# Kernel tuning notes

Hardware: AMD Instinct MI355X
Metric: run time of the kernel (lower is better)

Reference implementation:

```python
import jax, jax.numpy as jnp
import numpy as np

EPS = 1e-5
INF = 1e5


def setup_inputs() -> dict:
    key = jax.random.key(0)
    ks = iter(jax.random.split(key, 32))
    B, N, F, H, NH, C = 2, 384, 64, 64, 4, 32
    def lin(k, fi, fo):
        return jax.random.normal(k, (fi, fo), jnp.float32) / np.sqrt(fi).astype(np.float32)
    d = {}
    d['h'] = jax.random.normal(next(ks), (B, N, F), jnp.float32)
    d['x'] = jax.random.normal(next(ks), (B, N, 3), jnp.float32)
    # edge_model (ConcatenationFilter): Linear(2F+1,H), SiLU, Linear(H,H), SiLU
    d['We0'] = lin(next(ks), 2 * F + 1, H); d['be0'] = jnp.zeros(H, jnp.float32)
    d['We1'] = lin(next(ks), H, H);         d['be1'] = jnp.zeros(H, jnp.float32)
    # semantic_attention_mlp: Linear(H, n_heads), LeakyReLU(0.2)
    d['Ws'] = lin(next(ks), H, NH);         d['bs'] = jnp.zeros(NH, jnp.float32)
    # coefficients_mlp: Linear(H,H), SiLU, Linear(H,C)
    d['Wc0'] = lin(next(ks), H, H);         d['bc0'] = jnp.zeros(H, jnp.float32)
    d['Wc1'] = lin(next(ks), H, C);         d['bc1'] = jnp.zeros(C, jnp.float32)
    # post_norm_mlp: Linear(C,H), SiLU, Linear(H,H)
    d['Wp0'] = lin(next(ks), C, H);         d['bp0'] = jnp.zeros(H, jnp.float32)
    d['Wp1'] = lin(next(ks), H, H);         d['bp1'] = jnp.zeros(H, jnp.float32)
    # coordinate_mlp: Linear(H,H), SiLU, Linear(H,1,bias=False) init gain 1e-3
    d['Wx0'] = lin(next(ks), H, H);         d['bx0'] = jnp.zeros(H, jnp.float32)
    d['Wx1'] = lin(next(ks), H, 1) * 1e-3
    # node_mlp: Linear(NH*H + H + F, H), SiLU, Linear(H, F)
    d['Wn0'] = lin(next(ks), NH * H + H + F, H); d['bn0'] = jnp.zeros(H, jnp.float32)
    d['Wn1'] = lin(next(ks), H, F);         d['bn1'] = jnp.zeros(F, jnp.float32)
    d['log_gamma'] = jnp.zeros(NH, jnp.float32)
    return d


def _forward(h, x, We0, be0, We1, be1, Ws, bs, Wc0, bc0, Wc1, bc1,
             Wp0, bp0, Wp1, bp1, Wx0, bx0, Wx1, Wn0, bn0, Wn1, bn1, log_gamma):
    B, N, F = h.shape
    silu = jax.nn.silu

    # pairwise displacements and distances: (B,N,N,3), (B,N,N,1)
    x_minus_xt = x[:, :, None, :] - x[:, None, :, :]
    norm = jnp.sqrt(jnp.sum(x_minus_xt * x_minus_xt, axis=-1, keepdims=True) + EPS)

    # pairwise node-feature concat + distance -> edge MLP (ConcatenationFilter)
    hi = jnp.broadcast_to(h[:, :, None, :], (B, N, N, F))
    hj = jnp.broadcast_to(h[:, None, :, :], (B, N, N, F))
    e_in = jnp.concatenate([hi, hj, norm], axis=-1)           # (B,N,N,2F+1)
    h_e = silu(silu(e_in @ We0 + be0) @ We1 + be1)            # (B,N,N,H)

    eye = jnp.eye(N, dtype=h.dtype)[None, :, :, None]         # mask self-edges

    # euclidean attention per head, softmax over neighbors j (axis=-2)
    eu = jax.nn.softmax(-(norm + INF * eye) * jnp.exp(log_gamma), axis=-2)  # (B,N,N,NH)
    # semantic attention
    sem_logits = jax.nn.leaky_relu(h_e @ Ws + bs, 0.2) - INF * eye
    sem = jax.nn.softmax(sem_logits, axis=-2)                 # (B,N,N,NH)
    comb = eu * sem
    comb = comb / (jnp.sum(comb, axis=-2, keepdims=True) + EPS)

    # attention-weighted multi-head edge features, aggregated over neighbors
    h_e_att = (comb[..., :, None] * h_e[..., None, :]).reshape(B, N, N, -1)  # (B,N,N,NH*H)
    h_e_agg = jnp.sum(h_e_att, axis=-2)                       # (B,N,NH*H)

    # spatial attention: equivariant combinations of unit direction vectors
    coeff = silu(h_e @ Wc0 + bc0) @ Wc1 + bc1                 # (B,N,N,C)
    x_hat = x_minus_xt / (norm + EPS)                         # (B,N,N,3)
    combinations = coeff[..., :, None] * x_hat[..., None, :]  # (B,N,N,C,3)
    comb_sum = jnp.mean(combinations, axis=2)                 # mean over j -> (B,N,C,3)
    comb_norm = jnp.sum(comb_sum * comb_sum, axis=-1)         # (B,N,C)
    h_comb = silu(comb_norm @ Wp0 + bp0) @ Wp1 + bp1          # (B,N,H)

    # node update (residual)
    node_in = jnp.concatenate([h, h_e_agg, h_comb], axis=-1)
    h_out = h + (silu(node_in @ Wn0 + bn0) @ Wn1 + bn1)

    # coordinate update: scalar-gated displacements, mean over neighbors
    scale = silu(h_e @ Wx0 + bx0) @ Wx1                       # (B,N,N,1)
    x_out = x + jnp.mean(x_minus_xt * scale, axis=2)          # (B,N,3)
    return h_out, x_out


def reference(h, x, We0, be0, We1, be1, Ws, bs, Wc0, bc0, Wc1, bc1,
              Wp0, bp0, Wp1, bp1, Wx0, bx0, Wx1, Wn0, bn0, Wn1, bn1, log_gamma):
    return _forward(h, x, We0, be0, We1, be1, Ws, bs, Wc0, bc0, Wc1, bc1,
                    Wp0, bp0, Wp1, bp1, Wx0, bx0, Wx1, Wn0, bn0, Wn1, bn1, log_gamma)
```

## Files before the change

### kernel.cpp

```cpp
#include <hip/hip_runtime.h>

#define NPT 384
#define NB 2
#define HOFF 49152

typedef unsigned short u16;
typedef unsigned int u32;
typedef __bf16 bf16x8 __attribute__((ext_vector_type(8)));
typedef float f32x4 __attribute__((ext_vector_type(4)));

struct alignas(16) U4 { u32 x, y, z, w; };

constexpr float kEPS = 1e-5f;
constexpr float kINF = 1e5f;

__device__ __forceinline__ u16 f2b(float f) {
  u32 x = __float_as_uint(f);
  x += 0x7fffu + ((x >> 16) & 1u);
  return (u16)(x >> 16);
}
__device__ __forceinline__ float b2f(u32 u) { return __uint_as_float(u << 16); }
__device__ __forceinline__ float silu_f(float v) { return v / (1.f + __expf(-v)); }
__device__ __forceinline__ float wredmax(float v) {
#pragma unroll
  for (int m = 32; m >= 1; m >>= 1) v = fmaxf(v, __shfl_xor(v, m, 64));
  return v;
}
__device__ __forceinline__ float wredsum(float v) {
#pragma unroll
  for (int m = 32; m >= 1; m >>= 1) v += __shfl_xor(v, m, 64);
  return v;
}
__device__ __forceinline__ void up8(U4 u, float* f) {
  f[0] = b2f(u.x & 0xffffu); f[1] = b2f(u.x >> 16);
  f[2] = b2f(u.y & 0xffffu); f[3] = b2f(u.y >> 16);
  f[4] = b2f(u.z & 0xffffu); f[5] = b2f(u.z >> 16);
  f[6] = b2f(u.w & 0xffffu); f[7] = b2f(u.w >> 16);
}

__global__ __launch_bounds__(64) void sake_prep(
    const float* __restrict__ h, const float* __restrict__ We0,
    const float* __restrict__ be0, const float* __restrict__ We1,
    const float* __restrict__ Wc0, const float* __restrict__ Wc1,
    const float* __restrict__ Wx0, const float* __restrict__ Ws,
    float* __restrict__ U, float* __restrict__ V, u16* __restrict__ WT)
{
  const int t = threadIdx.x;
  const int blk = blockIdx.x;
  if (blk < NB * NPT) {
    __shared__ float hs[64];
    hs[t] = h[blk * 64 + t];
    __syncthreads();
    float u = be0[t], v = 0.f;
#pragma unroll 8
    for (int k = 0; k < 64; k++) {
      float hv = hs[k];
      u = fmaf(hv, We0[k * 64 + t], u);
      v = fmaf(hv, We0[(64 + k) * 64 + t], v);
    }
    U[blk * 64 + t] = u;
    V[blk * 64 + t] = v;
  } else {
    const int wsel = blk - NB * NPT;
    if (wsel == 4) {
      u16* dst = WT + 14336;
      for (int o = t; o < 16 * 64; o += 64) {
        int c = o >> 6, k = o & 63;
        dst[o] = (c < 4) ? f2b(Ws[k * 4 + c]) : (u16)0;
      }
      return;
    }
    const float* src; int nout; u16* dst;
    if      (wsel == 0) { src = We1; nout = 64; dst = WT;         }
    else if (wsel == 1) { src = Wc0; nout = 64; dst = WT + 4096;  }
    else if (wsel == 2) { src = Wx0; nout = 64; dst = WT + 8192;  }
    else                { src = Wc1; nout = 32; dst = WT + 12288; }
    const int total = 64 * nout;
    for (int o = t; o < total; o += 64) {
      int n = o >> 6, k = o & 63;
      dst[o] = f2b(src[k * nout + n]);
    }
  }
}

struct MainArgs {
  const float *h, *x, *U, *V;
  const u16 *We1T, *Wc0T, *Wx0T, *Wc1T, *WsPT;
  const float *We0, *bs, *be1, *bc0, *bc1, *bx0, *Wx1, *log_gamma;
  const float *Wp0, *bp0, *Wp1, *bp1, *Wn0, *bn0, *Wn1, *bn1;
  float* out;
};

template<bool DUALT>
__device__ __forceinline__ void gemm64(const u16* aT, const u16* __restrict__ wG,
                                       const float* bias, u16* oT, u16* oTT, int w, int lane)
{
  const int m0 = w << 4;
  const int arow = m0 + (lane & 15);
  const int r7 = arow & 7;
  const int kg = lane >> 4;
  bf16x8 a0 = *(const bf16x8*)(aT + arow * 64 + ((kg ^ r7) << 3));
  bf16x8 a1 = *(const bf16x8*)(aT + arow * 64 + ((((kg + 4)) ^ r7) << 3));
#pragma unroll
  for (int nt = 0; nt < 4; nt++) {
    const int col = (nt << 4) + (lane & 15);
    const u16* wrow = wG + col * 64;
    bf16x8 b0 = *(const bf16x8*)(wrow + (kg << 3));
    bf16x8 b1 = *(const bf16x8*)(wrow + 32 + (kg << 3));
    f32x4 acc = {0.f, 0.f, 0.f, 0.f};
    acc = __builtin_amdgcn_mfma_f32_16x16x32_bf16(a0, b0, acc, 0, 0, 0);
    acc = __builtin_amdgcn_mfma_f32_16x16x32_bf16(a1, b1, acc, 0, 0, 0);
    const float bv = bias[col];
    const int cs = col >> 3, ce = col & 7;
#pragma unroll
    for (int r = 0; r < 4; r++) {
      const int row = m0 + (kg << 2) + r;
      const u16 v = f2b(silu_f(acc[r] + bv));
      oT[row * 64 + ((cs ^ (row & 7)) << 3) + ce] = v;
      if constexpr (DUALT)
        oTT[col * 64 + ((((row >> 3)) ^ (col & 7)) << 3) + (row & 7)] = v;
    }
  }
}

__global__ __launch_bounds__(256, 3) void sake_main(MainArgs A)
{
  __shared__ __align__(16) u16 buf0[64 * 64];
  __shared__ __align__(16) u16 hes[64 * 64];
  __shared__ __align__(16) u16 hesT[64 * 64];
  __shared__ __align__(16) u16 E_lds[16 * 64];
  __shared__ __align__(16) u16 coeff[64 * 34];
  __shared__ float raw_lds[64 * 5];
  __shared__ float disp[64][3];
  __shared__ float nrm_s[64];
  __shared__ float invn_s[64];
  __shared__ float sU[64], wd[64], sbe1[64], sbc0[64], sbx0[64], sWx1[64];
  __shared__ float sbc1[32], sbs[4], sgam[4], xi_s[3];
  __shared__ float facL_s[4], coefh_s[4];
  __shared__ float node_in[384];
  __shared__ float t0s[64];
  __shared__ float cmv[96];

  const int t = threadIdx.x;
  const int w = t >> 6, lane = t & 63;
  const int bi = blockIdx.x;
  const int b = bi / NPT, i = bi - b * NPT;
  const int jj2 = t >> 2, q4 = t & 3;

  if (t < 64) {
    sU[t]   = A.U[bi * 64 + t];
    wd[t]   = A.We0[128 * 64 + t];
    sbe1[t] = A.be1[t];
    sbc0[t] = A.bc0[t];
    sbx0[t] = A.bx0[t];
    sWx1[t] = A.Wx1[t];
    if (t < 32) sbc1[t] = A.bc1[t];
    if (t < 4) { sbs[t] = A.bs[t]; sgam[t] = __expf(A.log_gamma[t]); }
    if (t < 3) xi_s[t] = A.x[(b * NPT + i) * 3 + t];
  }
  ((u32*)E_lds)[t] = 0; ((u32*)E_lds)[256 + t] = 0;
  __syncthreads();

  f32x4 aFrag = {0.f, 0.f, 0.f, 0.f};
  float mL = -1e30f, SL = 0.f, mb = -1e30f, Sb = 0.f, saPart = 0.f;
  float cA0 = 0, cA1 = 0, cA2 = 0, xA0 = 0, xA1 = 0, xA2 = 0;

  for (int jt = 0; jt < 6; ++jt) {
    const int j0 = jt << 6;
    __syncthreads();

    {
      const int j = j0 + jj2;
      const float* xp = &A.x[(b * NPT + j) * 3];
      float dx0 = xi_s[0] - xp[0], dx1 = xi_s[1] - xp[1], dx2 = xi_s[2] - xp[2];
      float nr = sqrtf(fmaf(dx0, dx0, fmaf(dx1, dx1, fmaf(dx2, dx2, kEPS))));
      if (q4 == 0) {
        disp[jj2][0] = dx0; disp[jj2][1] = dx1; disp[jj2][2] = dx2;
        nrm_s[jj2] = nr; invn_s[jj2] = 1.f / (nr + kEPS);
      }
      const float4* vp = (const float4*)(A.V + (size_t)(b * NPT + j) * 64 + q4 * 16);
      float4 v0_ = vp[0], v1_ = vp[1], v2_ = vp[2], v3_ = vp[3];
      float vv[16] = {v0_.x, v0_.y, v0_.z, v0_.w, v1_.x, v1_.y, v1_.z, v1_.w,
                      v2_.x, v2_.y, v2_.z, v2_.w, v3_.x, v3_.y, v3_.z, v3_.w};
      u16 pk[16];
#pragma unroll
      for (int e = 0; e < 16; e++) {
        const int f = q4 * 16 + e;
        pk[e] = f2b(silu_f(sU[f] + vv[e] + nr * wd[f]));
      }
      U4 lo, hi;
      lo.x = pk[0] | ((u32)pk[1] << 16);  lo.y = pk[2] | ((u32)pk[3] << 16);
      lo.z = pk[4] | ((u32)pk[5] << 16);  lo.w = pk[6] | ((u32)pk[7] << 16);
      hi.x = pk[8] | ((u32)pk[9] << 16);  hi.y = pk[10] | ((u32)pk[11] << 16);
      hi.z = pk[12] | ((u32)pk[13] << 16); hi.w = pk[14] | ((u32)pk[15] << 16);
      const int r7 = jj2 & 7;
      *(U4*)(buf0 + jj2 * 64 + (((q4 * 2) ^ r7) << 3)) = lo;
      *(U4*)(buf0 + jj2 * 64 + (((q4 * 2 + 1) ^ r7) << 3)) = hi;
    }
    gemm64<true>(buf0, A.We1T, sbe1, hes, hesT, w, lane);
    __syncthreads();

    gemm64<false>(hes, A.Wc0T, sbc0, buf0, nullptr, w, lane);
    {
      const int m0 = w << 4;
      const int arow = m0 + (lane & 15);
      const int r7a = arow & 7;
      const int kg = lane >> 4;
      bf16x8 a0 = *(const bf16x8*)(buf0 + arow * 64 + ((kg ^ r7a) << 3));
      bf16x8 a1 = *(const bf16x8*)(buf0 + arow * 64 + (((kg + 4) ^ r7a) << 3));
#pragma unroll
      for (int nt = 0; nt < 2; nt++) {
        const int col = (nt << 4) + (lane & 15);
        const u16* wrow = A.Wc1T + col * 64;
        bf16x8 b0 = *(const bf16x8*)(wrow + (kg << 3));
        bf16x8 b1 = *(const bf16x8*)(wrow + 32 + (kg << 3));
        f32x4 acc = {0.f, 0.f, 0.f, 0.f};
        acc = __builtin_amdgcn_mfma_f32_16x16x32_bf16(a0, b0, acc, 0, 0, 0);
        acc = __builtin_amdgcn_mfma_f32_16x16x32_bf16(a1, b1, acc, 0, 0, 0);
        const float bv = sbc1[col];
#pragma unroll
        for (int r = 0; r < 4; r++) {
          const int row = m0 + (kg << 2) + r;
          coeff[row * 34 + col] = f2b(acc[r] + bv);
        }
      }
    }
    {
      const int c = t & 31, g = t >> 5;
#pragma unroll
      for (int it = 0; it < 8; ++it) {
        const int jj = (g << 3) + it;
        const float s = b2f(coeff[jj * 34 + c]) * invn_s[jj];
        cA0 = fmaf(s, disp[jj][0], cA0);
        cA1 = fmaf(s, disp[jj][1], cA1);
        cA2 = fmaf(s, disp[jj][2], cA2);
      }
    }
    gemm64<false>(hes, A.Wx0T, sbx0, buf0, nullptr, w, lane);
    {
      const int jj = jj2;
      const int r7 = jj & 7;
      float acc = 0.f;
#pragma unroll
      for (int c2 = 0; c2 < 2; c2++) {
        const int c = q4 * 2 + c2;
        U4 u = *(const U4*)(buf0 + jj * 64 + ((c ^ r7) << 3));
        float f8[8]; up8(u, f8);
#pragma unroll
        for (int e = 0; e < 8; e++) acc = fmaf(f8[e], sWx1[c * 8 + e], acc);
      }
      acc += __shfl_xor(acc, 1, 64);
      acc += __shfl_xor(acc, 2, 64);
      if (q4 == 0) {
        xA0 = fmaf(disp[jj][0], acc, xA0);
        xA1 = fmaf(disp[jj][1], acc, xA1);
        xA2 = fmaf(disp[jj][2], acc, xA2);
      }
    }
    {
      const int m0 = w << 4;
      const int arow = m0 + (lane & 15);
      const int r7a = arow & 7;
      const int kg = lane >> 4;
      bf16x8 a0 = *(const bf16x8*)(hes + arow * 64 + ((kg ^ r7a) << 3));
      bf16x8 a1 = *(const bf16x8*)(hes + arow * 64 + (((kg + 4) ^ r7a) << 3));
      const u16* wrow = A.WsPT + (lane & 15) * 64;
      bf16x8 b0 = *(const bf16x8*)(wrow + (kg << 3));
      bf16x8 b1 = *(const bf16x8*)(wrow + 32 + (kg << 3));
      f32x4 acc = {0.f, 0.f, 0.f, 0.f};
      acc = __builtin_amdgcn_mfma_f32_16x16x32_bf16(a0, b0, acc, 0, 0, 0);
      acc = __builtin_amdgcn_mfma_f32_16x16x32_bf16(a1, b1, acc, 0, 0, 0);
      if ((lane & 15) < 4) {
#pragma unroll
        for (int r = 0; r < 4; r++)
          raw_lds[(m0 + (kg << 2) + r) * 5 + (lane & 15)] = acc[r];
      }
    }
    __syncthreads();

    {
      const int jj = lane, head = w;
      float raw = raw_lds[jj * 5 + head] + sbs[head];
      float bsem = (raw > 0.f) ? raw : 0.2f * raw;
      const bool self = (j0 + jj) == i;
      if (self) bsem -= kINF;
      const float aeu = -(nrm_s[jj] + (self ? kINF : 0.f)) * sgam[head];
      const float L = aeu + bsem;
      const float nmb = fmaxf(mb, wredmax(bsem));
      const float nmL = fmaxf(mL, wredmax(L));
      saPart += __expf(aeu);
      const float eB = __expf(bsem - nmb);
      const float eL = __expf(L - nmL);
      Sb = fmaf(Sb, __expf(mb - nmb), wredsum(eB));
      const float facL = __expf(mL - nmL);
      SL = fmaf(SL, facL, wredsum(eL));
      mb = nmb; mL = nmL;
      E_lds[head * 64 + (((jj >> 3) ^ head) << 3) + (jj & 7)] = f2b(eL);
      if (lane == 0) facL_s[head] = facL;
    }
    __syncthreads();

    {
      const int kg = lane >> 4;
      const int erow = lane & 15;
      const int e7 = erow & 7;
      bf16x8 ea0 = *(const bf16x8*)(E_lds + erow * 64 + ((kg ^ e7) << 3));
      bf16x8 ea1 = *(const bf16x8*)(E_lds + erow * 64 + (((kg + 4) ^ e7) << 3));
      const int f = (w << 4) + (lane & 15);
      const int f7 = f & 7;
      bf16x8 hb0 = *(const bf16x8*)(hesT + f * 64 + ((kg ^ f7) << 3));
      bf16x8 hb1 = *(const bf16x8*)(hesT + f * 64 + (((kg + 4) ^ f7) << 3));
#pragma unroll
      for (int r = 0; r < 4; r++) aFrag[r] *= facL_s[r];
      aFrag = __builtin_amdgcn_mfma_f32_16x16x32_bf16(ea0, hb0, aFrag, 0, 0, 0);
      aFrag = __builtin_amdgcn_mfma_f32_16x16x32_bf16(ea1, hb1, aFrag, 0, 0, 0);
    }
  }

  __syncthreads();
  float* scratch = (float*)coeff;
  float* xscr = (float*)hes;
  scratch[t * 3 + 0] = cA0; scratch[t * 3 + 1] = cA1; scratch[t * 3 + 2] = cA2;
  if (q4 == 0) { xscr[jj2 * 3 + 0] = xA0; xscr[jj2 * 3 + 1] = xA1; xscr[jj2 * 3 + 2] = xA2; }
  {
    const float Sa = wredsum(saPart);
    if (lane == 0) {
      const float Ff = __expf(mL - mb);
      const float denom = fmaf(SL, Ff, kEPS * Sa * Sb);
      coefh_s[w] = Ff / denom;
    }
  }
  if (t < 64) node_in[t] = A.h[bi * 64 + t];
  __syncthreads();
  if (lane < 16) {
#pragma unroll
    for (int r = 0; r < 4; r++)
      node_in[64 + r * 64 + (w << 4) + lane] = aFrag[r] * coefh_s[r];
  }
  if (t < 96) {
    const int c = t & 31, d = t >> 5;
    float s = 0.f;
#pragma unroll
    for (int g = 0; g < 8; g++) s += scratch[(g * 32 + c) * 3 + d];
    cmv[d * 32 + c] = s * (1.f / 384.f);
  }
  if (t >= 128 && t < 131) {
    const int d = t - 128;
    float s = 0.f;
    for (int k = 0; k < 64; k++) s += xscr[k * 3 + d];
    A.out[HOFF + bi * 3 + d] = xi_s[d] + s * (1.f / 384.f);
  }
  __syncthreads();
  if (t < 32) {
    float v0 = cmv[t], v1 = cmv[32 + t], v2 = cmv[64 + t];
    nrm_s[t] = v0 * v0 + v1 * v1 + v2 * v2;
  }
  __syncthreads();
  if (t < 64) {
    float acc = A.bp0[t];
    for (int c = 0; c < 32; c++) acc = fmaf(nrm_s[c], A.Wp0[c * 64 + t], acc);
    t0s[t] = silu_f(acc);
  }
  __syncthreads();
  if (t < 64) {
    float acc = A.bp1[t];
    for (int k = 0; k < 64; k++) acc = fmaf(t0s[k], A.Wp1[k * 64 + t], acc);
    node_in[320 + t] = acc;
  }
  __syncthreads();
  {
    const int f = t & 63, q = t >> 6;
    float acc = 0.f;
    const int k0 = q * 96;
    for (int k = 0; k < 96; k++) acc = fmaf(node_in[k0 + k], A.Wn0[(k0 + k) * 64 + f], acc);
    scratch[q * 64 + f] = acc;
  }
  __syncthreads();
  if (t < 64) {
    float s = scratch[t] + scratch[64 + t] + scratch[128 + t] + scratch[192 + t] + A.bn0[t];
    t0s[t] = silu_f(s);
  }
  __syncthreads();
  if (t < 64) {
    float acc = A.bn1[t];
    for (int k = 0; k < 64; k++) acc = fmaf(t0s[k], A.Wn1[k * 64 + t], acc);
    A.out[bi * 64 + t] = A.h[bi * 64 + t] + acc;
  }
}

extern "C" void kernel_launch(void* const* d_in, const int* in_sizes, int n_in,
                              void* d_out, int out_size, void* d_ws, size_t ws_size,
                              hipStream_t stream)
{
  (void)in_sizes; (void)n_in; (void)out_size; (void)ws_size;
  const float* h   = (const float*)d_in[0];
  const float* x   = (const float*)d_in[1];
  const float* We0 = (const float*)d_in[2];
  const float* be0 = (const float*)d_in[3];
  const float* We1 = (const float*)d_in[4];
  const float* be1 = (const float*)d_in[5];
  const float* Ws  = (const float*)d_in[6];
  const float* bs  = (const float*)d_in[7];
  const float* Wc0 = (const float*)d_in[8];
  const float* bc0 = (const float*)d_in[9];
  const float* Wc1 = (const float*)d_in[10];
  const float* bc1 = (const float*)d_in[11];
  const float* Wp0 = (const float*)d_in[12];
  const float* bp0 = (const float*)d_in[13];
  const float* Wp1 = (const float*)d_in[14];
  const float* bp1 = (const float*)d_in[15];
  const float* Wx0 = (const float*)d_in[16];
  const float* bx0 = (const float*)d_in[17];
  const float* Wx1 = (const float*)d_in[18];
  const float* Wn0 = (const float*)d_in[19];
  const float* bn0 = (const float*)d_in[20];
  const float* Wn1 = (const float*)d_in[21];
  const float* bn1 = (const float*)d_in[22];
  const float* lg  = (const float*)d_in[23];

  float* U = (float*)d_ws;
  float* V = U + NB * NPT * 64;
  u16* WT = (u16*)(V + NB * NPT * 64);

  sake_prep<<<NB * NPT + 5, 64, 0, stream>>>(h, We0, be0, We1, Wc0, Wc1, Wx0, Ws, U, V, WT);

  MainArgs A;
  A.h = h; A.x = x; A.U = U; A.V = V;
  A.We1T = WT; A.Wc0T = WT + 4096; A.Wx0T = WT + 8192; A.Wc1T = WT + 12288;
  A.WsPT = WT + 14336;
  A.We0 = We0; A.bs = bs; A.be1 = be1; A.bc0 = bc0; A.bc1 = bc1;
  A.bx0 = bx0; A.Wx1 = Wx1; A.log_gamma = lg;
  A.Wp0 = Wp0; A.bp0 = bp0; A.Wp1 = Wp1; A.bp1 = bp1;
  A.Wn0 = Wn0; A.bn0 = bn0; A.Wn1 = Wn1; A.bn1 = bn1;
  A.out = (float*)d_out;

  sake_main<<<NB * NPT, 256, 0, stream>>>(A);
}
```

Before: 118.6 us.

## Split neighbor tiles across blocks with partial softmax records and merge kernel

Instead of each block looping over all six 64-neighbor tiles for one node, each block now processes a single (node, tile) pair and writes partial attention sums, softmax max/sum statistics, coefficient and coordinate partials to a workspace record. A new merge kernel combines the per-tile records with log-sum-exp rescaling and runs the post-norm and node MLPs. This raises grid size sixfold and drops LDS use so more blocks fit per CU, at the cost of an extra launch, global round-trips for partials, and repeated per-block setup. It also switches to hardware bf16 conversion and rcp-based SiLU.

```diff
diff --git a/kernel.cpp b/kernel.cpp
--- a/kernel.cpp
+++ b/kernel.cpp
@@ -2,7 +2,11 @@
 
 #define NPT 384
 #define NB 2
+#define NROW (NB*NPT)
+#define NT 6
 #define HOFF 49152
+#define RECB 1024
+#define REC_OFF 424960
 
 typedef unsigned short u16;
 typedef unsigned int u32;
@@ -14,13 +18,10 @@
 constexpr float kEPS = 1e-5f;
 constexpr float kINF = 1e5f;
 
-__device__ __forceinline__ u16 f2b(float f) {
-  u32 x = __float_as_uint(f);
-  x += 0x7fffu + ((x >> 16) & 1u);
-  return (u16)(x >> 16);
-}
+__device__ __forceinline__ u16 f2b(float f) { __bf16 b = (__bf16)f; return __builtin_bit_cast(u16, b); }
+__device__ __forceinline__ u32 pk2(float lo, float hi) { return (u32)f2b(lo) | ((u32)f2b(hi) << 16); }
 __device__ __forceinline__ float b2f(u32 u) { return __uint_as_float(u << 16); }
-__device__ __forceinline__ float silu_f(float v) { return v / (1.f + __expf(-v)); }
+__device__ __forceinline__ float silu_f(float v) { return v * __builtin_amdgcn_rcpf(1.f + __expf(-v)); }
 __device__ __forceinline__ float wredmax(float v) {
 #pragma unroll
   for (int m = 32; m >= 1; m >>= 1) v = fmaxf(v, __shfl_xor(v, m, 64));
@@ -47,7 +48,7 @@
 {
   const int t = threadIdx.x;
   const int blk = blockIdx.x;
-  if (blk < NB * NPT) {
+  if (blk < NROW) {
     __shared__ float hs[64];
     hs[t] = h[blk * 64 + t];
     __syncthreads();
@@ -61,7 +62,7 @@
     U[blk * 64 + t] = u;
     V[blk * 64 + t] = v;
   } else {
-    const int wsel = blk - NB * NPT;
+    const int wsel = blk - NROW;
     if (wsel == 4) {
       u16* dst = WT + 14336;
       for (int o = t; o < 16 * 64; o += 64) {
@@ -84,11 +85,10 @@
 }
 
 struct MainArgs {
-  const float *h, *x, *U, *V;
+  const float *x, *U, *V;
   const u16 *We1T, *Wc0T, *Wx0T, *Wc1T, *WsPT;
   const float *We0, *bs, *be1, *bc0, *bc1, *bx0, *Wx1, *log_gamma;
-  const float *Wp0, *bp0, *Wp1, *bp1, *Wn0, *bn0, *Wn1, *bn1;
-  float* out;
+  char* rec;
 };
 
 template<bool DUALT>
@@ -123,29 +123,35 @@
   }
 }
 
-__global__ __launch_bounds__(256, 3) void sake_main(MainArgs A)
+__global__ __launch_bounds__(256, 5) void sake_main(MainArgs A)
 {
   __shared__ __align__(16) u16 buf0[64 * 64];
   __shared__ __align__(16) u16 hes[64 * 64];
   __shared__ __align__(16) u16 hesT[64 * 64];
-  __shared__ __align__(16) u16 E_lds[16 * 64];
-  __shared__ __align__(16) u16 coeff[64 * 34];
+  __shared__ __align__(16) u16 reg3[64 * 32];
   __shared__ float raw_lds[64 * 5];
   __shared__ float disp[64][3];
   __shared__ float nrm_s[64];
-  __shared__ float invn_s[64];
   __shared__ float sU[64], wd[64], sbe1[64], sbc0[64], sbx0[64], sWx1[64];
-  __shared__ float sbc1[32], sbs[4], sgam[4], xi_s[3];
-  __shared__ float facL_s[4], coefh_s[4];
-  __shared__ float node_in[384];
-  __shared__ float t0s[64];
-  __shared__ float cmv[96];
+  __shared__ float sbc1[32], sbs[4], sgam[4];
 
   const int t = threadIdx.x;
   const int w = t >> 6, lane = t & 63;
-  const int bi = blockIdx.x;
-  const int b = bi / NPT, i = bi - b * NPT;
+  const int bt = blockIdx.x;
+  const int i = bt % NPT;
+  const int bj = bt / NPT;
+  const int jt = bj % NT, b = bj / NT;
+  const int bi = b * NPT + i;
+  const int j0 = jt << 6;
   const int jj2 = t >> 2, q4 = t & 3;
+  char* rec = A.rec + (size_t)(bi * NT + jt) * RECB;
+
+  const int j = j0 + jj2;
+  const float* xp = &A.x[(b * NPT + j) * 3];
+  const float xj0 = xp[0], xj1 = xp[1], xj2 = xp[2];
+  const float xi0 = A.x[bi * 3 + 0], xi1 = A.x[bi * 3 + 1], xi2 = A.x[bi * 3 + 2];
+  const float4* vp = (const float4*)(A.V + (size_t)(b * NPT + j) * 64 + q4 * 16);
+  const float4 v0_ = vp[0], v1_ = vp[1], v2_ = vp[2], v3_ = vp[3];
 
   if (t < 64) {
     sU[t]   = A.U[bi * 64 + t];
@@ -156,235 +162,276 @@
     sWx1[t] = A.Wx1[t];
     if (t < 32) sbc1[t] = A.bc1[t];
     if (t < 4) { sbs[t] = A.bs[t]; sgam[t] = __expf(A.log_gamma[t]); }
-    if (t < 3) xi_s[t] = A.x[(b * NPT + i) * 3 + t];
-  }
-  ((u32*)E_lds)[t] = 0; ((u32*)E_lds)[256 + t] = 0;
-  __syncthreads();
-
-  f32x4 aFrag = {0.f, 0.f, 0.f, 0.f};
-  float mL = -1e30f, SL = 0.f, mb = -1e30f, Sb = 0.f, saPart = 0.f;
+  }
+  __syncthreads();
+
   float cA0 = 0, cA1 = 0, cA2 = 0, xA0 = 0, xA1 = 0, xA2 = 0;
 
-  for (int jt = 0; jt < 6; ++jt) {
-    const int j0 = jt << 6;
-    __syncthreads();
-
-    {
-      const int j = j0 + jj2;
-      const float* xp = &A.x[(b * NPT + j) * 3];
-      float dx0 = xi_s[0] - xp[0], dx1 = xi_s[1] - xp[1], dx2 = xi_s[2] - xp[2];
-      float nr = sqrtf(fmaf(dx0, dx0, fmaf(dx1, dx1, fmaf(dx2, dx2, kEPS))));
-      if (q4 == 0) {
-        disp[jj2][0] = dx0; disp[jj2][1] = dx1; disp[jj2][2] = dx2;
-        nrm_s[jj2] = nr; invn_s[jj2] = 1.f / (nr + kEPS);
-      }
-      const float4* vp = (const float4*)(A.V + (size_t)(b * NPT + j) * 64 + q4 * 16);
-      float4 v0_ = vp[0], v1_ = vp[1], v2_ = vp[2], v3_ = vp[3];
-      float vv[16] = {v0_.x, v0_.y, v0_.z, v0_.w, v1_.x, v1_.y, v1_.z, v1_.w,
-                      v2_.x, v2_.y, v2_.z, v2_.w, v3_.x, v3_.y, v3_.z, v3_.w};
-      u16 pk[16];
-#pragma unroll
-      for (int e = 0; e < 16; e++) {
-        const int f = q4 * 16 + e;
-        pk[e] = f2b(silu_f(sU[f] + vv[e] + nr * wd[f]));
-      }
-      U4 lo, hi;
-      lo.x = pk[0] | ((u32)pk[1] << 16);  lo.y = pk[2] | ((u32)pk[3] << 16);
-      lo.z = pk[4] | ((u32)pk[5] << 16);  lo.w = pk[6] | ((u32)pk[7] << 16);
-      hi.x = pk[8] | ((u32)pk[9] << 16);  hi.y = pk[10] | ((u32)pk[11] << 16);
-      hi.z = pk[12] | ((u32)pk[13] << 16); hi.w = pk[14] | ((u32)pk[15] << 16);
-      const int r7 = jj2 & 7;
-      *(U4*)(buf0 + jj2 * 64 + (((q4 * 2) ^ r7) << 3)) = lo;
-      *(U4*)(buf0 + jj2 * 64 + (((q4 * 2 + 1) ^ r7) << 3)) = hi;
-    }
-    gemm64<true>(buf0, A.We1T, sbe1, hes, hesT, w, lane);
-    __syncthreads();
-
-    gemm64<false>(hes, A.Wc0T, sbc0, buf0, nullptr, w, lane);
-    {
-      const int m0 = w << 4;
-      const int arow = m0 + (lane & 15);
-      const int r7a = arow & 7;
-      const int kg = lane >> 4;
-      bf16x8 a0 = *(const bf16x8*)(buf0 + arow * 64 + ((kg ^ r7a) << 3));
-      bf16x8 a1 = *(const bf16x8*)(buf0 + arow * 64 + (((kg + 4) ^ r7a) << 3));
-#pragma unroll
-      for (int nt = 0; nt < 2; nt++) {
-        const int col = (nt << 4) + (lane & 15);
-        const u16* wrow = A.Wc1T + col * 64;
-        bf16x8 b0 = *(const bf16x8*)(wrow + (kg << 3));
-        bf16x8 b1 = *(const bf16x8*)(wrow + 32 + (kg << 3));
-        f32x4 acc = {0.f, 0.f, 0.f, 0.f};
-        acc = __builtin_amdgcn_mfma_f32_16x16x32_bf16(a0, b0, acc, 0, 0, 0);
-        acc = __builtin_amdgcn_mfma_f32_16x16x32_bf16(a1, b1, acc, 0, 0, 0);
-        const float bv = sbc1[col];
-#pragma unroll
-        for (int r = 0; r < 4; r++) {
-          const int row = m0 + (kg << 2) + r;
-          coeff[row * 34 + col] = f2b(acc[r] + bv);
-        }
-      }
-    }
-    {
-      const int c = t & 31, g = t >> 5;
-#pragma unroll
-      for (int it = 0; it < 8; ++it) {
-        const int jj = (g << 3) + it;
-        const float s = b2f(coeff[jj * 34 + c]) * invn_s[jj];
-        cA0 = fmaf(s, disp[jj][0], cA0);
-        cA1 = fmaf(s, disp[jj][1], cA1);
-        cA2 = fmaf(s, disp[jj][2], cA2);
-      }
-    }
-    gemm64<false>(hes, A.Wx0T, sbx0, buf0, nullptr, w, lane);
-    {
-      const int jj = jj2;
-      const int r7 = jj & 7;
-      float acc = 0.f;
-#pragma unroll
-      for (int c2 = 0; c2 < 2; c2++) {
-        const int c = q4 * 2 + c2;
-        U4 u = *(const U4*)(buf0 + jj * 64 + ((c ^ r7) << 3));
-        float f8[8]; up8(u, f8);
-#pragma unroll
-        for (int e = 0; e < 8; e++) acc = fmaf(f8[e], sWx1[c * 8 + e], acc);
-      }
-      acc += __shfl_xor(acc, 1, 64);
-      acc += __shfl_xor(acc, 2, 64);
-      if (q4 == 0) {
-        xA0 = fmaf(disp[jj][0], acc, xA0);
-        xA1 = fmaf(disp[jj][1], acc, xA1);
-        xA2 = fmaf(disp[jj][2], acc, xA2);
-      }
-    }
-    {
-      const int m0 = w << 4;
-      const int arow = m0 + (lane & 15);
-      const int r7a = arow & 7;
-      const int kg = lane >> 4;
-      bf16x8 a0 = *(const bf16x8*)(hes + arow * 64 + ((kg ^ r7a) << 3));
-      bf16x8 a1 = *(const bf16x8*)(hes + arow * 64 + (((kg + 4) ^ r7a) << 3));
-      const u16* wrow = A.WsPT + (lane & 15) * 64;
+  {
+    float dx0 = xi0 - xj0, dx1 = xi1 - xj1, dx2 = xi2 - xj2;
+    float nr = sqrtf(fmaf(dx0, dx0, fmaf(dx1, dx1, fmaf(dx2, dx2, kEPS))));
+    if (q4 == 0) { disp[jj2][0] = dx0; disp[jj2][1] = dx1; disp[jj2][2] = dx2; nrm_s[jj2] = nr; }
+    float vv[16] = {v0_.x, v0_.y, v0_.z, v0_.w, v1_.x, v1_.y, v1_.z, v1_.w,
+                    v2_.x, v2_.y, v2_.z, v2_.w, v3_.x, v3_.y, v3_.z, v3_.w};
+    float sv[16];
+#pragma unroll
+    for (int e = 0; e < 16; e++) {
+      const int f = q4 * 16 + e;
+      sv[e] = silu_f(sU[f] + vv[e] + nr * wd[f]);
+    }
+    U4 lo, hi;
+    lo.x = pk2(sv[0], sv[1]);   lo.y = pk2(sv[2], sv[3]);
+    lo.z = pk2(sv[4], sv[5]);   lo.w = pk2(sv[6], sv[7]);
+    hi.x = pk2(sv[8], sv[9]);   hi.y = pk2(sv[10], sv[11]);
+    hi.z = pk2(sv[12], sv[13]); hi.w = pk2(sv[14], sv[15]);
+    const int r7 = jj2 & 7;
+    *(U4*)(buf0 + jj2 * 64 + (((q4 * 2) ^ r7) << 3)) = lo;
+    *(U4*)(buf0 + jj2 * 64 + (((q4 * 2 + 1) ^ r7) << 3)) = hi;
+  }
+  gemm64<true>(buf0, A.We1T, sbe1, hes, hesT, w, lane);
+  gemm64<false>(hes, A.Wc0T, sbc0, buf0, nullptr, w, lane);
+  {
+    const int m0 = w << 4;
+    const int arow = m0 + (lane & 15);
+    const int r7a = arow & 7;
+    const int kg = lane >> 4;
+    bf16x8 a0 = *(const bf16x8*)(buf0 + arow * 64 + ((kg ^ r7a) << 3));
+    bf16x8 a1 = *(const bf16x8*)(buf0 + arow * 64 + (((kg + 4) ^ r7a) << 3));
+#pragma unroll
+    for (int nt = 0; nt < 2; nt++) {
+      const int col = (nt << 4) + (lane & 15);
+      const u16* wrow = A.Wc1T + col * 64;
       bf16x8 b0 = *(const bf16x8*)(wrow + (kg << 3));
       bf16x8 b1 = *(const bf16x8*)(wrow + 32 + (kg << 3));
       f32x4 acc = {0.f, 0.f, 0.f, 0.f};
       acc = __builtin_amdgcn_mfma_f32_16x16x32_bf16(a0, b0, acc, 0, 0, 0);
       acc = __builtin_amdgcn_mfma_f32_16x16x32_bf16(a1, b1, acc, 0, 0, 0);
-      if ((lane & 15) < 4) {
-#pragma unroll
-        for (int r = 0; r < 4; r++)
-          raw_lds[(m0 + (kg << 2) + r) * 5 + (lane & 15)] = acc[r];
+      const float bv = sbc1[col];
+#pragma unroll
+      for (int r = 0; r < 4; r++) {
+        const int row = m0 + (kg << 2) + r;
+        reg3[row * 32 + col] = f2b(acc[r] + bv);
       }
     }
-    __syncthreads();
-
-    {
-      const int jj = lane, head = w;
-      float raw = raw_lds[jj * 5 + head] + sbs[head];
-      float bsem = (raw > 0.f) ? raw : 0.2f * raw;
-      const bool self = (j0 + jj) == i;
-      if (self) bsem -= kINF;
-      const float aeu = -(nrm_s[jj] + (self ? kINF : 0.f)) * sgam[head];
-      const float L = aeu + bsem;
-      const float nmb = fmaxf(mb, wredmax(bsem));
-      const float nmL = fmaxf(mL, wredmax(L));
-      saPart += __expf(aeu);
-      const float eB = __expf(bsem - nmb);
-      const float eL = __expf(L - nmL);
-      Sb = fmaf(Sb, __expf(mb - nmb), wredsum(eB));
-      const float facL = __expf(mL - nmL);
-      SL = fmaf(SL, facL, wredsum(eL));
-      mb = nmb; mL = nmL;
-      E_lds[head * 64 + (((jj >> 3) ^ head) << 3) + (jj & 7)] = f2b(eL);
-      if (lane == 0) facL_s[head] = facL;
-    }
-    __syncthreads();
-
-    {
-      const int kg = lane >> 4;
-      const int erow = lane & 15;
-      const int e7 = erow & 7;
-      bf16x8 ea0 = *(const bf16x8*)(E_lds + erow * 64 + ((kg ^ e7) << 3));
-      bf16x8 ea1 = *(const bf16x8*)(E_lds + erow * 64 + (((kg + 4) ^ e7) << 3));
-      const int f = (w << 4) + (lane & 15);
-      const int f7 = f & 7;
-      bf16x8 hb0 = *(const bf16x8*)(hesT + f * 64 + ((kg ^ f7) << 3));
-      bf16x8 hb1 = *(const bf16x8*)(hesT + f * 64 + (((kg + 4) ^ f7) << 3));
-#pragma unroll
-      for (int r = 0; r < 4; r++) aFrag[r] *= facL_s[r];
-      aFrag = __builtin_amdgcn_mfma_f32_16x16x32_bf16(ea0, hb0, aFrag, 0, 0, 0);
-      aFrag = __builtin_amdgcn_mfma_f32_16x16x32_bf16(ea1, hb1, aFrag, 0, 0, 0);
-    }
-  }
-
-  __syncthreads();
-  float* scratch = (float*)coeff;
-  float* xscr = (float*)hes;
-  scratch[t * 3 + 0] = cA0; scratch[t * 3 + 1] = cA1; scratch[t * 3 + 2] = cA2;
-  if (q4 == 0) { xscr[jj2 * 3 + 0] = xA0; xscr[jj2 * 3 + 1] = xA1; xscr[jj2 * 3 + 2] = xA2; }
-  {
-    const float Sa = wredsum(saPart);
+  }
+  {
+    const int c = t & 31, g = t >> 5;
+#pragma unroll
+    for (int it = 0; it < 8; ++it) {
+      const int jj = (g << 3) + it;
+      const float s = b2f(reg3[jj * 32 + c]) * __builtin_amdgcn_rcpf(nrm_s[jj] + kEPS);
+      cA0 = fmaf(s, disp[jj][0], cA0);
+      cA1 = fmaf(s, disp[jj][1], cA1);
+      cA2 = fmaf(s, disp[jj][2], cA2);
+    }
+  }
+  gemm64<false>(hes, A.Wx0T, sbx0, buf0, nullptr, w, lane);
+  {
+    const int jj = jj2;
+    const int r7 = jj & 7;
+    float acc = 0.f;
+#pragma unroll
+    for (int c2 = 0; c2 < 2; c2++) {
+      const int c = q4 * 2 + c2;
+      U4 u = *(const U4*)(buf0 + jj * 64 + ((c ^ r7) << 3));
+      float f8[8]; up8(u, f8);
+#pragma unroll
+      for (int e = 0; e < 8; e++) acc = fmaf(f8[e], sWx1[c * 8 + e], acc);
+    }
+    acc += __shfl_xor(acc, 1, 64);
+    acc += __shfl_xor(acc, 2, 64);
+    if (q4 == 0) {
+      xA0 = fmaf(disp[jj][0], acc, xA0);
+      xA1 = fmaf(disp[jj][1], acc, xA1);
+      xA2 = fmaf(disp[jj][2], acc, xA2);
+    }
+  }
+  {
+    const int m0 = w << 4;
+    const int arow = m0 + (lane & 15);
+    const int r7a = arow & 7;
+    const int kg = lane >> 4;
+    bf16x8 a0 = *(const bf16x8*)(hes + arow * 64 + ((kg ^ r7a) << 3));
+    bf16x8 a1 = *(const bf16x8*)(hes + arow * 64 + (((kg + 4) ^ r7a) << 3));
+    const u16* wrow = A.WsPT + (lane & 15) * 64;
+    bf16x8 b0 = *(const bf16x8*)(wrow + (kg << 3));
+    bf16x8 b1 = *(const bf16x8*)(wrow + 32 + (kg << 3));
+    f32x4 acc = {0.f, 0.f, 0.f, 0.f};
+    acc = __builtin_amdgcn_mfma_f32_16x16x32_bf16(a0, b0, acc, 0, 0, 0);
+    acc = __builtin_amdgcn_mfma_f32_16x16x32_bf16(a1, b1, acc, 0, 0, 0);
+    if ((lane & 15) < 4) {
+#pragma unroll
+      for (int r = 0; r < 4; r++)
+        raw_lds[(m0 + (kg << 2) + r) * 5 + (lane & 15)] = acc[r];
+    }
+  }
+  __syncthreads();
+
+  float* cascr = (float*)hes;
+  cascr[t * 3 + 0] = cA0; cascr[t * 3 + 1] = cA1; cascr[t * 3 + 2] = cA2;
+  if (q4 == 0) {
+    float* xs = (float*)hes + 768;
+    xs[jj2 * 3 + 0] = xA0; xs[jj2 * 3 + 1] = xA1; xs[jj2 * 3 + 2] = xA2;
+  }
+  {
+    const int jj = lane, head = w;
+    float raw = raw_lds[jj * 5 + head] + sbs[head];
+    float bsem = (raw > 0.f) ? raw : 0.2f * raw;
+    const bool self = (j0 + jj) == i;
+    if (self) bsem -= kINF;
+    const float aeu = -(nrm_s[jj] + (self ? kINF : 0.f)) * sgam[head];
+    const float L = aeu + bsem;
+    const float mL = wredmax(L);
+    const float eL = __expf(L - mL);
+    const float SL = wredsum(eL);
+    const float mb = wredmax(bsem);
+    const float Sb = wredsum(__expf(bsem - mb));
+    const float Sa = wredsum(__expf(aeu));
+    u16* E = reg3 + 1024;
+    E[head * 64 + (((jj >> 3) ^ head) << 3) + (jj & 7)] = f2b(eL);
     if (lane == 0) {
-      const float Ff = __expf(mL - mb);
-      const float denom = fmaf(SL, Ff, kEPS * Sa * Sb);
-      coefh_s[w] = Ff / denom;
-    }
-  }
-  if (t < 64) node_in[t] = A.h[bi * 64 + t];
-  __syncthreads();
-  if (lane < 16) {
-#pragma unroll
-    for (int r = 0; r < 4; r++)
-      node_in[64 + r * 64 + (w << 4) + lane] = aFrag[r] * coefh_s[r];
+      float* sp = (float*)(rec + 908) + head * 5;
+      sp[0] = mL; sp[1] = SL; sp[2] = mb; sp[3] = Sb; sp[4] = Sa;
+    }
+  }
+  __syncthreads();
+
+  {
+    const int kg = lane >> 4;
+    const int erow = lane & 15;
+    const int e7 = erow & 7;
+    const u16* E = reg3 + 1024;
+    bf16x8 ea0 = *(const bf16x8*)(E + erow * 64 + ((kg ^ e7) << 3));
+    bf16x8 ea1 = *(const bf16x8*)(E + erow * 64 + (((kg + 4) ^ e7) << 3));
+    const int f = (w << 4) + (lane & 15);
+    const int f7 = f & 7;
+    bf16x8 hb0 = *(const bf16x8*)(hesT + f * 64 + ((kg ^ f7) << 3));
+    bf16x8 hb1 = *(const bf16x8*)(hesT + f * 64 + (((kg + 4) ^ f7) << 3));
+    f32x4 aF = {0.f, 0.f, 0.f, 0.f};
+    aF = __builtin_amdgcn_mfma_f32_16x16x32_bf16(ea0, hb0, aF, 0, 0, 0);
+    aF = __builtin_amdgcn_mfma_f32_16x16x32_bf16(ea1, hb1, aF, 0, 0, 0);
+    if (kg == 0) {
+      u16* rA = (u16*)rec;
+#pragma unroll
+      for (int r = 0; r < 4; r++) rA[r * 64 + (w << 4) + (lane & 15)] = f2b(aF[r]);
+    }
   }
   if (t < 96) {
     const int c = t & 31, d = t >> 5;
     float s = 0.f;
 #pragma unroll
-    for (int g = 0; g < 8; g++) s += scratch[(g * 32 + c) * 3 + d];
-    cmv[d * 32 + c] = s * (1.f / 384.f);
+    for (int g = 0; g < 8; g++) s += cascr[(g * 32 + c) * 3 + d];
+    ((float*)(rec + 512))[d * 32 + c] = s;
+  } else if (t < 99) {
+    const int d = t - 96;
+    float s = 0.f;
+    for (int k = 0; k < 64; k++) s += ((float*)hes + 768)[k * 3 + d];
+    ((float*)(rec + 896))[d] = s;
+  }
+}
+
+struct MergeArgs {
+  const float *h, *x, *Wp0, *bp0, *Wp1, *bp1, *Wn0, *bn0, *Wn1, *bn1;
+  const char* rec;
+  float* out;
+};
+
+__global__ __launch_bounds__(256) void sake_merge(MergeArgs M)
+{
+  __shared__ float sc[NT][20];
+  __shared__ float wAl[NT][4];
+  __shared__ float coefh[4];
+  __shared__ float node_in[384];
+  __shared__ float cmv[96];
+  __shared__ float nrm32[32];
+  __shared__ float t0s[64];
+  __shared__ float scr[256];
+
+  const int t = threadIdx.x;
+  const int bi = blockIdx.x;
+  const char* rb = M.rec + (size_t)bi * NT * RECB;
+
+  if (t < NT * 20) {
+    const int tt = t / 20, k = t % 20;
+    sc[tt][k] = ((const float*)(rb + tt * RECB + 908))[k];
+  }
+  if (t < 64) node_in[t] = M.h[bi * 64 + t];
+  __syncthreads();
+  if (t < 4) {
+    const int hh = t;
+    float mL = -1e30f, mb = -1e30f;
+    for (int tt = 0; tt < NT; tt++) {
+      mL = fmaxf(mL, sc[tt][hh * 5 + 0]);
+      mb = fmaxf(mb, sc[tt][hh * 5 + 2]);
+    }
+    float SL = 0.f, Sb = 0.f, Sa = 0.f;
+    for (int tt = 0; tt < NT; tt++) {
+      const float wa = __expf(sc[tt][hh * 5 + 0] - mL);
+      wAl[tt][hh] = wa;
+      SL = fmaf(wa, sc[tt][hh * 5 + 1], SL);
+      Sb = fmaf(__expf(sc[tt][hh * 5 + 2] - mb), sc[tt][hh * 5 + 3], Sb);
+      Sa += sc[tt][hh * 5 + 4];
+    }
+    const float Ff = __expf(mL - mb);
+    coefh[hh] = Ff / fmaf(SL, Ff, kEPS * Sa * Sb);
+  }
+  __syncthreads();
+  {
+    const int hh = t >> 6, f = t & 63;
+    float s = 0.f;
+#pragma unroll
+    for (int tt = 0; tt < NT; tt++)
+      s = fmaf(wAl[tt][hh], b2f(((const u16*)(rb + tt * RECB))[hh * 64 + f]), s);
+    node_in[64 + hh * 64 + f] = s * coefh[hh];
+  }
+  if (t < 96) {
+    float s = 0.f;
+#pragma unroll
+    for (int tt = 0; tt < NT; tt++) s += ((const float*)(rb + tt * RECB + 512))[t];
+    cmv[t] = s * (1.f / 384.f);
   }
   if (t >= 128 && t < 131) {
     const int d = t - 128;
     float s = 0.f;
-    for (int k = 0; k < 64; k++) s += xscr[k * 3 + d];
-    A.out[HOFF + bi * 3 + d] = xi_s[d] + s * (1.f / 384.f);
+#pragma unroll
+    for (int tt = 0; tt < NT; tt++) s += ((const float*)(rb + tt * RECB + 896))[d];
+    M.out[HOFF + bi * 3 + d] = M.x[bi * 3 + d] + s * (1.f / 384.f);
   }
   __syncthreads();
   if (t < 32) {
-    float v0 = cmv[t], v1 = cmv[32 + t], v2 = cmv[64 + t];
-    nrm_s[t] = v0 * v0 + v1 * v1 + v2 * v2;
+    const float v0 = cmv[t], v1 = cmv[32 + t], v2 = cmv[64 + t];
+    nrm32[t] = v0 * v0 + v1 * v1 + v2 * v2;
   }
   __syncthreads();
   if (t < 64) {
-    float acc = A.bp0[t];
-    for (int c = 0; c < 32; c++) acc = fmaf(nrm_s[c], A.Wp0[c * 64 + t], acc);
-    t0s[t] = silu_f(acc);
+    float a = M.bp0[t];
+    for (int c = 0; c < 32; c++) a = fmaf(nrm32[c], M.Wp0[c * 64 + t], a);
+    t0s[t] = silu_f(a);
   }
   __syncthreads();
   if (t < 64) {
-    float acc = A.bp1[t];
-    for (int k = 0; k < 64; k++) acc = fmaf(t0s[k], A.Wp1[k * 64 + t], acc);
-    node_in[320 + t] = acc;
+    float a = M.bp1[t];
+    for (int k = 0; k < 64; k++) a = fmaf(t0s[k], M.Wp1[k * 64 + t], a);
+    node_in[320 + t] = a;
   }
   __syncthreads();
   {
     const int f = t & 63, q = t >> 6;
-    float acc = 0.f;
+    float a = 0.f;
     const int k0 = q * 96;
-    for (int k = 0; k < 96; k++) acc = fmaf(node_in[k0 + k], A.Wn0[(k0 + k) * 64 + f], acc);
-    scratch[q * 64 + f] = acc;
+    for (int k = 0; k < 96; k++) a = fmaf(node_in[k0 + k], M.Wn0[(k0 + k) * 64 + f], a);
+    scr[t] = a;
   }
   __syncthreads();
   if (t < 64) {
-    float s = scratch[t] + scratch[64 + t] + scratch[128 + t] + scratch[192 + t] + A.bn0[t];
+    const float s = scr[t] + scr[64 + t] + scr[128 + t] + scr[192 + t] + M.bn0[t];
     t0s[t] = silu_f(s);
   }
   __syncthreads();
   if (t < 64) {
-    float acc = A.bn1[t];
-    for (int k = 0; k < 64; k++) acc = fmaf(t0s[k], A.Wn1[k * 64 + t], acc);
-    A.out[bi * 64 + t] = A.h[bi * 64 + t] + acc;
+    float a = M.bn1[t];
+    for (int k = 0; k < 64; k++) a = fmaf(t0s[k], M.Wn1[k * 64 + t], a);
+    M.out[bi * 64 + t] = M.h[bi * 64 + t] + a;
   }
 }
 
@@ -419,20 +466,25 @@
   const float* lg  = (const float*)d_in[23];
 
   float* U = (float*)d_ws;
-  float* V = U + NB * NPT * 64;
-  u16* WT = (u16*)(V + NB * NPT * 64);
-
-  sake_prep<<<NB * NPT + 5, 64, 0, stream>>>(h, We0, be0, We1, Wc0, Wc1, Wx0, Ws, U, V, WT);
+  float* V = U + NROW * 64;
+  u16* WT = (u16*)(V + NROW * 64);
+  char* rec = (char*)d_ws + REC_OFF;
+
+  sake_prep<<<NROW + 5, 64, 0, stream>>>(h, We0, be0, We1, Wc0, Wc1, Wx0, Ws, U, V, WT);
 
   MainArgs A;
-  A.h = h; A.x = x; A.U = U; A.V = V;
+  A.x = x; A.U = U; A.V = V;
   A.We1T = WT; A.Wc0T = WT + 4096; A.Wx0T = WT + 8192; A.Wc1T = WT + 12288;
   A.WsPT = WT + 14336;
   A.We0 = We0; A.bs = bs; A.be1 = be1; A.bc0 = bc0; A.bc1 = bc1;
   A.bx0 = bx0; A.Wx1 = Wx1; A.log_gamma = lg;
-  A.Wp0 = Wp0; A.bp0 = bp0; A.Wp1 = Wp1; A.bp1 = bp1;
-  A.Wn0 = Wn0; A.bn0 = bn0; A.Wn1 = Wn1; A.bn1 = bn1;
-  A.out = (float*)d_out;
-
-  sake_main<<<NB * NPT, 256, 0, stream>>>(A);
-}
+  A.rec = rec;
+  sake_main<<<NROW * NT, 256, 0, stream>>>(A);
+
+  MergeArgs Mg;
+  Mg.h = h; Mg.x = x;
+  Mg.Wp0 = Wp0; Mg.bp0 = bp0; Mg.Wp1 = Wp1; Mg.bp1 = bp1;
+  Mg.Wn0 = Wn0; Mg.bn0 = bn0; Mg.Wn1 = Wn1; Mg.bn1 = bn1;
+  Mg.rec = rec; Mg.out = (float*)d_out;
+  sake_merge<<<NROW, 256, 0, stream>>>(Mg);
+}
```

Result: faster. 98.15 us (-17.3%).
